# Performance work log

Measured on AMD Instinct MI355X. Metric: run time of the kernel, lower is better.

## Reference

```python
import jax, jax.numpy as jnp
import numpy as np

N = 100000   # nodes
E = 600000   # edges
D = 128      # hidden_dim
R = 8        # edge_vocab_size (num_relations)
B = 64       # graphs in batch
V = 5000     # node_vocab_size
L = 3        # num_layers


def setup_inputs() -> dict:
    key = jax.random.key(0)
    ks = jax.random.split(key, 16)
    s = 1.0 / np.sqrt(D)
    node_type = jax.random.randint(ks[0], (N,), 0, V, dtype=jnp.int32)
    edge_index = jax.random.randint(ks[1], (2, E), 0, N, dtype=jnp.int32)
    edge_type = jax.random.randint(ks[2], (E,), 0, R, dtype=jnp.int32)
    batch = jnp.sort(jax.random.randint(ks[3], (N,), 0, B, dtype=jnp.int32))
    node_emb = jax.random.normal(ks[4], (V, D), dtype=jnp.float32)
    rel_w = jax.random.normal(ks[5], (L, R, D, D), dtype=jnp.float32) * s
    root_w = jax.random.normal(ks[6], (L, D, D), dtype=jnp.float32) * s
    bias = jnp.zeros((L, D), dtype=jnp.float32)
    risk_w1 = jax.random.normal(ks[7], (D, D), dtype=jnp.float32) * s
    risk_b1 = jnp.zeros((D,), dtype=jnp.float32)
    risk_w2 = jax.random.normal(ks[8], (D, 1), dtype=jnp.float32) * s
    risk_b2 = jnp.zeros((1,), dtype=jnp.float32)
    safe_w1 = jax.random.normal(ks[9], (D, D), dtype=jnp.float32) * s
    safe_b1 = jnp.zeros((D,), dtype=jnp.float32)
    safe_w2 = jax.random.normal(ks[10], (D, 1), dtype=jnp.float32) * s
    safe_b2 = jnp.zeros((1,), dtype=jnp.float32)
    return dict(node_type=node_type, edge_index=edge_index, edge_type=edge_type,
                batch=batch, node_emb=node_emb, rel_w=rel_w, root_w=root_w,
                bias=bias, risk_w1=risk_w1, risk_b1=risk_b1, risk_w2=risk_w2,
                risk_b2=risk_b2, safe_w1=safe_w1, safe_b1=safe_b1,
                safe_w2=safe_w2, safe_b2=safe_b2)


def _rgcn_layer(x, edge_index, edge_type, Wrel, Wroot, b):
    # PyG RGCNConv: per-relation mean aggregation of source features,
    # then relation-specific linear + root transform + bias.
    src, dst = edge_index[0], edge_index[1]
    seg = dst * R + edge_type                      # combined (node, relation) id
    msgs = x[src]                                  # [E, D] gather
    sums = jax.ops.segment_sum(msgs, seg, num_segments=N * R)      # [N*R, D]
    cnt = jax.ops.segment_sum(jnp.ones((E,), x.dtype), seg, num_segments=N * R)
    mean = sums / jnp.maximum(cnt, 1.0)[:, None]
    mean = mean.reshape(N, R, D)
    out = jnp.einsum('nrd,rde->ne', mean, Wrel) + x @ Wroot + b
    return out


def _mlp_head(g, w1, b1, w2, b2):
    h = jax.nn.relu(g @ w1 + b1)
    return (h @ w2 + b2).squeeze(-1)               # dropout is identity in eval


def reference(node_type, edge_index, edge_type, batch, node_emb, rel_w, root_w,
              bias, risk_w1, risk_b1, risk_w2, risk_b2, safe_w1, safe_b1,
              safe_w2, safe_b2):
    x = node_emb[node_type]                        # [N, D]
    for l in range(L):                             # fixed small layer loop
        x = jax.nn.relu(_rgcn_layer(x, edge_index, edge_type,
                                    rel_w[l], root_w[l], bias[l]))
    # global_mean_pool over graph ids
    g_sum = jax.ops.segment_sum(x, batch, num_segments=B)          # [B, D]
    g_cnt = jax.ops.segment_sum(jnp.ones((N,), x.dtype), batch, num_segments=B)
    g = g_sum / jnp.maximum(g_cnt, 1.0)[:, None]
    risk_pred = _mlp_head(g, risk_w1, risk_b1, risk_w2, risk_b2)   # [B]
    safe_logit = _mlp_head(g, safe_w1, safe_b1, safe_w2, safe_b2)  # [B]
    return risk_pred, safe_logit
```

## Files before the change

kernel.cpp:

```cpp
#include <hip/hip_runtime.h>
#include <hip/hip_bf16.h>

#define N_NODES 100000
#define N_EDGES 600000
#define DIM     128
#define N_REL   8
#define N_GRAPH 64
#define N_LAYER 3
#define NR      (N_NODES * N_REL)
#define NB1     782

typedef __attribute__((ext_vector_type(4))) float float4v;
typedef __attribute__((ext_vector_type(2))) float float2v;
typedef unsigned long long ull;

__device__ __forceinline__ int gswz8(int row, int g) {
    return row * 16 + (g ^ (row & 15));
}

#define W8_TOTAL (N_LAYER * 9 * 8192)
#define PB_HIST  2344
#define PB_GATH  12500
#define PB_WPRE  864
#define PB_BCNT  1
#define PB_TOTAL (PB_HIST + PB_GATH + PB_WPRE + PB_BCNT)

__global__ __launch_bounds__(256) void k_prep(
    const int* __restrict__ ei, const int* __restrict__ et, int* __restrict__ counts,
    const int* __restrict__ nt, const float* __restrict__ emb, unsigned int* __restrict__ x8,
    const float* __restrict__ relw, const float* __restrict__ rootw,
    unsigned short* __restrict__ W8,
    const int* __restrict__ batch, int* __restrict__ gcnt)
{
    const int b = blockIdx.x, t = threadIdx.x;
    if (b < PB_HIST) {
        int e = b * 256 + t;
        if (e < N_EDGES) {
            int seg = ei[N_EDGES + e] * N_REL + et[e];
            atomicAdd(&counts[seg], 1);
        }
    } else if (b < PB_HIST + PB_GATH) {
        int gid = (b - PB_HIST) * 256 + t;
        int n = gid >> 5, up = gid & 31;
        const float* row = emb + (size_t)nt[n] * DIM;
        int p0 = up * 4;
        float f0 = row[((p0 + 0) & 7) * 16 + ((p0 + 0) >> 3)];
        float f1 = row[((p0 + 1) & 7) * 16 + ((p0 + 1) >> 3)];
        float f2 = row[((p0 + 2) & 7) * 16 + ((p0 + 2) >> 3)];
        float f3 = row[((p0 + 3) & 7) * 16 + ((p0 + 3) >> 3)];
        int u = __builtin_amdgcn_cvt_pk_fp8_f32(f0, f1, 0, false);
        u = __builtin_amdgcn_cvt_pk_fp8_f32(f2, f3, u, true);
        x8[gid] = (unsigned int)u;
    } else if (b < PB_HIST + PB_GATH + PB_WPRE) {
        int gid = (b - PB_HIST - PB_GATH) * 256 + t;
        int l = gid / (9 * 8192);
        int rem = gid - l * 9 * 8192;
        int r = rem >> 13;
        int idx = rem & 8191;
        int n = idx >> 6, p2 = idx & 63;
        int pos0 = 2 * p2, pos1 = 2 * p2 + 1;
        int k0 = (pos0 & 7) * 16 + (pos0 >> 3);
        int k1 = (pos1 & 7) * 16 + (pos1 >> 3);
        float w0, w1;
        if (r < 8) {
            const float* base = relw + ((size_t)(l * 8 + r) * 128) * 128 + n;
            w0 = base[(size_t)k0 * 128];
            w1 = base[(size_t)k1 * 128];
        } else {
            const float* base = rootw + (size_t)l * 128 * 128 + n;
            w0 = base[(size_t)k0 * 128];
            w1 = base[(size_t)k1 * 128];
        }
        int pk = __builtin_amdgcn_cvt_pk_fp8_f32(w0, w1, 0, false);
        W8[gid] = (unsigned short)(pk & 0xffff);
    } else {
        int g = t;
        if (g < N_GRAPH) {
            int lo = 0, hi = N_NODES;
            while (lo < hi) { int mid = (lo + hi) >> 1; if (batch[mid] < g) lo = mid + 1; else hi = mid; }
            int start = lo;
            lo = 0; hi = N_NODES;
            while (lo < hi) { int mid = (lo + hi) >> 1; if (batch[mid] < g + 1) lo = mid + 1; else hi = mid; }
            gcnt[g] = lo - start;
        }
    }
}

__global__ __launch_bounds__(256) void k_scan1(const int* __restrict__ cnts,
                                               int* __restrict__ part,
                                               int* __restrict__ bsum) {
    __shared__ int sh[256];
    int t = threadIdx.x;
    int base = blockIdx.x * 1024 + t * 4;
    int v0 = (base + 0 < NR) ? cnts[base + 0] : 0;
    int v1 = (base + 1 < NR) ? cnts[base + 1] : 0;
    int v2 = (base + 2 < NR) ? cnts[base + 2] : 0;
    int v3 = (base + 3 < NR) ? cnts[base + 3] : 0;
    int tot = v0 + v1 + v2 + v3;
    sh[t] = tot;
    __syncthreads();
    for (int off = 1; off < 256; off <<= 1) {
        int x = (t >= off) ? sh[t - off] : 0;
        __syncthreads();
        sh[t] += x;
        __syncthreads();
    }
    int exc = sh[t] - tot;
    if (base + 0 < NR) part[base + 0] = exc;
    if (base + 1 < NR) part[base + 1] = exc + v0;
    if (base + 2 < NR) part[base + 2] = exc + v0 + v1;
    if (base + 3 < NR) part[base + 3] = exc + v0 + v1 + v2;
    if (t == 255) bsum[blockIdx.x] = sh[t];
}

__global__ __launch_bounds__(1024) void k_scan2(int* __restrict__ bsum, int nb) {
    __shared__ int sh[1024];
    int t = threadIdx.x;
    int v = (t < nb) ? bsum[t] : 0;
    sh[t] = v;
    __syncthreads();
    for (int off = 1; off < 1024; off <<= 1) {
        int x = (t >= off) ? sh[t - off] : 0;
        __syncthreads();
        sh[t] += x;
        __syncthreads();
    }
    if (t < nb) bsum[t] = sh[t] - v;
}

__global__ void k_scan3(const int* __restrict__ part, const int* __restrict__ bsum,
                        int* __restrict__ rowptr, int* __restrict__ cursor) {
    int i = blockIdx.x * 256 + threadIdx.x;
    if (i < NR) {
        int v = part[i] + bsum[i >> 10];
        rowptr[i] = v;
        cursor[i] = v;
    }
    if (i == 0) rowptr[NR] = N_EDGES;
}

__global__ void k_scatter(const int* __restrict__ ei, const int* __restrict__ et,
                          int* __restrict__ cursor, int* __restrict__ srcs) {
    int e = blockIdx.x * 256 + threadIdx.x;
    if (e < N_EDGES) {
        int seg = ei[N_EDGES + e] * N_REL + et[e];
        int p = atomicAdd(&cursor[seg], 1);
        srcs[p] = ei[e];
    }
}

#define BM2 128
__global__ __launch_bounds__(256, 2) void k_gemm(
    const unsigned int* __restrict__ x8in,
    unsigned int* __restrict__ x8out,
    const unsigned short* __restrict__ W8,
    const float* __restrict__ bias,
    const int* __restrict__ rowptr,
    const int* __restrict__ srcs)
{
    __shared__ __align__(16) ull Bls[4096];
    __shared__ __align__(16) ull Als[2048];
    const int t = threadIdx.x;
    const int wv = t >> 6, lane = t & 63;
    const int quad = lane >> 4, l15 = lane & 15;
    const int oct = lane >> 3, h = lane & 7;
    const int m0 = blockIdx.x * BM2;
    const int gn = m0 + wv * 32 + (lane >> 1);
    const int f = lane & 1;

    float4v acc[2][8];
#pragma unroll
    for (int nt = 0; nt < 8; ++nt) {
        float bc = bias[nt * 16 + l15];
        acc[0][nt] = (float4v){bc, bc, bc, bc};
        acc[1][nt] = (float4v){bc, bc, bc, bc};
    }

    const ull* Xr = (const ull*)x8in;
    const uint4* x4p = (const uint4*)x8in;
    ull* AlsW = Als + wv * 512;
    uint4* Als4 = (uint4*)AlsW;

    ull bR[8], aR[8];
    uint4 u0[4], u1[4];
    int cc[4], eb[4], s2v[4], s3v[4];

#define ACCUM(U) do {                                                  \
        A0 += __builtin_amdgcn_cvt_pk_f32_fp8((int)(U).x, false);      \
        A1 += __builtin_amdgcn_cvt_pk_f32_fp8((int)(U).x, true);       \
        A2 += __builtin_amdgcn_cvt_pk_f32_fp8((int)(U).y, false);      \
        A3 += __builtin_amdgcn_cvt_pk_f32_fp8((int)(U).y, true);       \
        A4 += __builtin_amdgcn_cvt_pk_f32_fp8((int)(U).z, false);      \
        A5 += __builtin_amdgcn_cvt_pk_f32_fp8((int)(U).z, true);       \
        A6 += __builtin_amdgcn_cvt_pk_f32_fp8((int)(U).w, false);      \
        A7 += __builtin_amdgcn_cvt_pk_f32_fp8((int)(U).w, true);       \
    } while (0)

    auto rp_load = [&](int rr) -> int {
        int idxp = (gn < N_NODES) ? gn * 8 + rr + f : NR;
        return rowptr[idxp];
    };
    auto src_load = [&](int val, int& s0, int& s2) {
        int e0l = __shfl(val, lane & 62);
        int cl  = __shfl(val, lane | 1) - e0l;
        s0 = (f < cl) ? srcs[e0l + f] : 0;
        s2 = (f + 2 < cl) ? srcs[e0l + 2 + f] : 0;
    };
    auto gat_issue = [&](int val, int sl0, int sl2) {
#pragma unroll
        for (int nn = 0; nn < 4; ++nn) {
            int lw = nn * 8 + oct;
            int e0 = __shfl(val, lw * 2);
            int e1 = __shfl(val, lw * 2 + 1);
            cc[nn] = e1 - e0; eb[nn] = e0;
            int s0 = __shfl(sl0, lw * 2);
            int s1 = __shfl(sl0, lw * 2 + 1);
            s2v[nn] = __shfl(sl2, lw * 2);
            s3v[nn] = __shfl(sl2, lw * 2 + 1);
            if (cc[nn] > 0) u0[nn] = x4p[(size_t)s0 * 8 + h];
            if (cc[nn] > 1) u1[nn] = x4p[(size_t)s1 * 8 + h];
        }
    };
    auto agg_consume = [&]() {
        uint4 u2[4], u3[4];
#pragma unroll
        for (int nn = 0; nn < 4; ++nn) {
            if (cc[nn] > 2) u2[nn] = x4p[(size_t)s2v[nn] * 8 + h];
            if (cc[nn] > 3) u3[nn] = x4p[(size_t)s3v[nn] * 8 + h];
        }
#pragma unroll
        for (int nn = 0; nn < 4; ++nn) {
            int lw = nn * 8 + oct;
            float2v A0 = {0.f, 0.f}, A1 = {0.f, 0.f}, A2 = {0.f, 0.f}, A3 = {0.f, 0.f};
            float2v A4 = {0.f, 0.f}, A5 = {0.f, 0.f}, A6 = {0.f, 0.f}, A7 = {0.f, 0.f};
            if (cc[nn] > 0) ACCUM(u0[nn]);
            if (cc[nn] > 1) ACCUM(u1[nn]);
            if (cc[nn] > 2) ACCUM(u2[nn]);
            if (cc[nn] > 3) ACCUM(u3[nn]);
#pragma unroll 1
            for (int k = 4; k < cc[nn]; ++k) {
                int s = srcs[eb[nn] + k];
                uint4 uu = x4p[(size_t)s * 8 + h];
                ACCUM(uu);
            }
            float inv = (cc[nn] > 0) ? 1.0f / (float)cc[nn] : 0.f;
            float2v iv = {inv, inv};
            A0 *= iv; A1 *= iv; A2 *= iv; A3 *= iv;
            A4 *= iv; A5 *= iv; A6 *= iv; A7 *= iv;
            int w0 = __builtin_amdgcn_cvt_pk_fp8_f32(A0.x, A0.y, 0, false);
            w0 = __builtin_amdgcn_cvt_pk_fp8_f32(A1.x, A1.y, w0, true);
            int w1 = __builtin_amdgcn_cvt_pk_fp8_f32(A2.x, A2.y, 0, false);
            w1 = __builtin_amdgcn_cvt_pk_fp8_f32(A3.x, A3.y, w1, true);
            int w2 = __builtin_amdgcn_cvt_pk_fp8_f32(A4.x, A4.y, 0, false);
            w2 = __builtin_amdgcn_cvt_pk_fp8_f32(A5.x, A5.y, w2, true);
            int w3 = __builtin_amdgcn_cvt_pk_fp8_f32(A6.x, A6.y, 0, false);
            w3 = __builtin_amdgcn_cvt_pk_fp8_f32(A7.x, A7.y, w3, true);
            uint4 w; w.x = (unsigned int)w0; w.y = (unsigned int)w1;
            w.z = (unsigned int)w2; w.w = (unsigned int)w3;
            Als4[(lw >> 4) * 128 + h * 16 + ((lw & 15) ^ h)] = w;
        }
    };

    {
        const ull* Wc = (const ull*)W8;
#pragma unroll
        for (int i = 0; i < 8; ++i) bR[i] = Wc[t + 256 * i];
    }
    int vS3 = rp_load(0);
    int vS2 = rp_load(1);
    int vNew = rp_load(2);
    int sl0A, sl2A, sl0N, sl2N;
    src_load(vS3, sl0A, sl2A);
    gat_issue(vS3, sl0A, sl2A);
    src_load(vS2, sl0A, sl2A);
    agg_consume();
    vS3 = vS2; vS2 = vNew;
#pragma unroll
    for (int i = 0; i < 8; ++i) {
        int idx = t + 256 * i;
        Bls[gswz8(idx >> 4, idx & 15)] = bR[i];
    }
    __syncthreads();

#pragma unroll
    for (int c = 0; c < 9; ++c) {
        const int cur = (c & 1) * 2048;
        if (c <= 4) vNew = rp_load(c + 3);
        if (c <= 5) src_load(vS2, sl0N, sl2N);
        if (c <= 6) gat_issue(vS3, sl0A, sl2A);
        if (c < 8) {
            const ull* Wc = (const ull*)(W8 + (size_t)(c + 1) * 8192);
#pragma unroll
            for (int i = 0; i < 8; ++i) bR[i] = Wc[t + 256 * i];
        }
        if (c == 7) {
#pragma unroll
            for (int i = 0; i < 8; ++i) {
                int rt = i >> 2, kk = i & 3;
                aR[i] = Xr[(size_t)(m0 + wv * 32 + rt * 16 + l15) * 16 + kk * 4 + quad];
            }
        }
#pragma unroll
        for (int kk = 0; kk < 4; ++kk) {
            long long a0, a1;
            if (c == 8) {
                a0 = (long long)aR[kk];
                a1 = (long long)aR[4 + kk];
            } else {
                int j4 = kk * 4 + quad;
                int h2 = j4 >> 1, hf = j4 & 1;
                int slot = ((h2 * 16 + (l15 ^ h2)) << 1) | hf;
                a0 = (long long)AlsW[slot];
                a1 = (long long)AlsW[256 + slot];
            }
            int g = kk * 4 + quad;
#pragma unroll
            for (int nt = 0; nt < 8; ++nt) {
                long long b8 = (long long)Bls[cur + (nt * 16 + l15) * 16 + (g ^ l15)];
                acc[0][nt] = __builtin_amdgcn_mfma_f32_16x16x32_fp8_fp8(a0, b8, acc[0][nt], 0, 0, 0);
                acc[1][nt] = __builtin_amdgcn_mfma_f32_16x16x32_fp8_fp8(a1, b8, acc[1][nt], 0, 0, 0);
            }
        }
        if (c <= 6) agg_consume();
        if (c < 8) {
            const int nxt = ((c + 1) & 1) * 2048;
#pragma unroll
            for (int i = 0; i < 8; ++i) {
                int idx = t + 256 * i;
                Bls[nxt + gswz8(idx >> 4, idx & 15)] = bR[i];
            }
            __syncthreads();
        }
        vS3 = vS2; vS2 = vNew; sl0A = sl0N; sl2A = sl2N;
    }
#undef ACCUM

    ull* outs = (ull*)x8out;
#pragma unroll
    for (int rt = 0; rt < 2; ++rt) {
#pragma unroll
        for (int i = 0; i < 4; ++i) {
            int row = m0 + wv * 32 + rt * 16 + quad * 4 + i;
            float v0 = acc[rt][0][i], v1 = acc[rt][1][i];
            float v2 = acc[rt][2][i], v3 = acc[rt][3][i];
            float v4 = acc[rt][4][i], v5 = acc[rt][5][i];
            float v6 = acc[rt][6][i], v7 = acc[rt][7][i];
            v0 = v0 > 0.f ? v0 : 0.f;  v1 = v1 > 0.f ? v1 : 0.f;
            v2 = v2 > 0.f ? v2 : 0.f;  v3 = v3 > 0.f ? v3 : 0.f;
            v4 = v4 > 0.f ? v4 : 0.f;  v5 = v5 > 0.f ? v5 : 0.f;
            v6 = v6 > 0.f ? v6 : 0.f;  v7 = v7 > 0.f ? v7 : 0.f;
            int lo = __builtin_amdgcn_cvt_pk_fp8_f32(v0, v1, 0, false);
            lo = __builtin_amdgcn_cvt_pk_fp8_f32(v2, v3, lo, true);
            int hi = __builtin_amdgcn_cvt_pk_fp8_f32(v4, v5, 0, false);
            hi = __builtin_amdgcn_cvt_pk_fp8_f32(v6, v7, hi, true);
            if (row < N_NODES) {
                ull w = ((ull)(unsigned int)hi << 32) | (unsigned int)lo;
                outs[(size_t)row * 16 + l15] = w;
            }
        }
    }
}

__global__ __launch_bounds__(256) void k_pool(const unsigned int* __restrict__ x8,
                                              const int* __restrict__ batch,
                                              float* __restrict__ gsum) {
    const int wv = threadIdx.x >> 6, lane = threadIdx.x & 63;
    const int n0 = (blockIdx.x * 4 + wv) * 64;
    if (n0 >= N_NODES) return;
    int n1 = n0 + 64;
    if (n1 > N_NODES) n1 = N_NODES;
    const int nb = n1 - n0;
    const unsigned short* xs = (const unsigned short*)x8;
    int bb = batch[n0 + (lane < nb ? lane : nb - 1)];
    float2v A = {0.f, 0.f};
    int cur = __shfl(bb, 0);
    for (int base = 0; base < nb; base += 8) {
        unsigned int u[8];
        int m = nb - base;
#pragma unroll
        for (int qq = 0; qq < 8; ++qq)
            if (qq < m) u[qq] = xs[(size_t)(n0 + base + qq) * 64 + lane];
#pragma unroll
        for (int qq = 0; qq < 8; ++qq) {
            if (qq < m) {
                int b = __shfl(bb, base + qq);
                if (b != cur) {
                    atomicAdd(&gsum[cur * 128 + lane * 2], A.x);
                    atomicAdd(&gsum[cur * 128 + lane * 2 + 1], A.y);
                    A = (float2v){0.f, 0.f};
                    cur = b;
                }
                A += __builtin_amdgcn_cvt_pk_f32_fp8((int)u[qq], false);
            }
        }
    }
    atomicAdd(&gsum[cur * 128 + lane * 2], A.x);
    atomicAdd(&gsum[cur * 128 + lane * 2 + 1], A.y);
}

__global__ __launch_bounds__(128) void k_heads(
    const float* __restrict__ gsum, const int* __restrict__ gcnt,
    const float* __restrict__ rw1, const float* __restrict__ rb1,
    const float* __restrict__ rw2, const float* __restrict__ rb2,
    const float* __restrict__ sw1, const float* __restrict__ sb1,
    const float* __restrict__ sw2, const float* __restrict__ sb2,
    float* __restrict__ out) {
    __shared__ float g[128];
    __shared__ float parts[2];
    int b = blockIdx.x, t = threadIdx.x;
    int c = gcnt[b];
    float invc = 1.0f / (float)(c > 0 ? c : 1);
    g[((t & 7) << 4) | (t >> 3)] = gsum[b * 128 + t] * invc;
    __syncthreads();
    float acc = rb1[t];
    for (int d = 0; d < 128; ++d) acc += g[d] * rw1[d * 128 + t];
    float h = acc > 0.f ? acc : 0.f;
    float p = h * rw2[t];
    for (int o = 32; o > 0; o >>= 1) p += __shfl_down(p, o);
    if ((t & 63) == 0) parts[t >> 6] = p;
    __syncthreads();
    if (t == 0) out[b] = parts[0] + parts[1] + rb2[0];
    __syncthreads();
    acc = sb1[t];
    for (int d = 0; d < 128; ++d) acc += g[d] * sw1[d * 128 + t];
    h = acc > 0.f ? acc : 0.f;
    p = h * sw2[t];
    for (int o = 32; o > 0; o >>= 1) p += __shfl_down(p, o);
    if ((t & 63) == 0) parts[t >> 6] = p;
    __syncthreads();
    if (t == 0) out[64 + b] = parts[0] + parts[1] + sb2[0];
}

extern "C" void kernel_launch(void* const* d_in, const int* in_sizes, int n_in,
                              void* d_out, int out_size, void* d_ws, size_t ws_size,
                              hipStream_t stream) {
    const int*   node_type  = (const int*)d_in[0];
    const int*   edge_index = (const int*)d_in[1];
    const int*   edge_type  = (const int*)d_in[2];
    const int*   batch      = (const int*)d_in[3];
    const float* node_emb   = (const float*)d_in[4];
    const float* rel_w      = (const float*)d_in[5];
    const float* root_w     = (const float*)d_in[6];
    const float* bias       = (const float*)d_in[7];
    const float* rw1        = (const float*)d_in[8];
    const float* rb1        = (const float*)d_in[9];
    const float* rw2        = (const float*)d_in[10];
    const float* rb2        = (const float*)d_in[11];
    const float* sw1        = (const float*)d_in[12];
    const float* sb1        = (const float*)d_in[13];
    const float* sw2        = (const float*)d_in[14];
    const float* sb2        = (const float*)d_in[15];
    float* out = (float*)d_out;

    char* ws = (char*)d_ws;
    size_t off = 0;
    auto alloc = [&](size_t bytes) -> void* {
        void* p = ws + off;
        off += (bytes + 255) & ~(size_t)255;
        return p;
    };
    unsigned int*   x8a    = (unsigned int*)alloc((size_t)N_NODES * 32 * 4);
    unsigned int*   x8b    = (unsigned int*)alloc((size_t)N_NODES * 32 * 4);
    int*            rowptr = (int*)alloc((size_t)(NR + 1) * 4);
    int*            srcs   = (int*)alloc((size_t)N_EDGES * 4);
    int*            bsum   = (int*)alloc(1024 * 4);
    unsigned short* W8     = (unsigned short*)alloc((size_t)W8_TOTAL * 2);
    float*          gsum   = (float*)alloc((64 * 128 + 64) * 4);
    int*            gcnt   = (int*)(gsum + 64 * 128);
    int*            cursor = (int*)alloc((size_t)NR * 4);
    int*            counts = (int*)alloc((size_t)NR * 4);
    if (off > ws_size) return;

    hipMemsetAsync(counts, 0, (size_t)NR * 4, stream);
    hipMemsetAsync(gsum, 0, (size_t)(64 * 128 + 64) * 4, stream);
    k_prep<<<PB_TOTAL, 256, 0, stream>>>(edge_index, edge_type, counts,
                                         node_type, node_emb, x8a,
                                         rel_w, root_w, W8, batch, gcnt);
    k_scan1<<<NB1, 256, 0, stream>>>(counts, cursor, bsum);
    k_scan2<<<1, 1024, 0, stream>>>(bsum, NB1);
    k_scan3<<<(NR + 255) / 256, 256, 0, stream>>>(cursor, bsum, rowptr, cursor);
    k_scatter<<<(N_EDGES + 255) / 256, 256, 0, stream>>>(edge_index, edge_type, cursor, srcs);

    unsigned int* xcur = x8a;
    unsigned int* xnext = x8b;
    const int gb = (N_NODES + BM2 - 1) / BM2;
    for (int l = 0; l < N_LAYER; ++l) {
        const unsigned short* W8l = W8 + (size_t)l * 9 * 8192;
        const float* bl = bias + (size_t)l * 128;
        k_gemm<<<gb, 256, 0, stream>>>(xcur, xnext, W8l, bl, rowptr, srcs);
        unsigned int* tmp = xcur; xcur = xnext; xnext = tmp;
    }

    k_pool<<<(N_NODES + 255) / 256, 256, 0, stream>>>(xcur, batch, gsum);
    k_heads<<<64, 128, 0, stream>>>(gsum, gcnt, rw1, rb1, rw2, rb2,
                                    sw1, sb1, sw2, sb2, out);
}
```

Measured before the change: 388.3 us.

## Load FP8 weights directly into registers in MFMA fragment order, drop LDS staging

The weight prep kernel now writes each relation or root FP8 matrix already permuted into per-lane MFMA B-fragment order. The GEMM kernel reads those fragments straight from global memory (L2) into double-buffered registers, one k-step ahead, instead of staging them through a swizzled LDS double buffer with a barrier per chunk. This removes the LDS writes and reads and the block-wide __syncthreads in the weight path. In exchange every wave reloads the same weights from global or cache, which raises L2 traffic and register pressure under the 2-blocks-per-CU launch bound.

```diff
diff --git a/kernel.cpp b/kernel.cpp
--- a/kernel.cpp
+++ b/kernel.cpp
@@ -13,10 +13,6 @@
 typedef __attribute__((ext_vector_type(4))) float float4v;
 typedef __attribute__((ext_vector_type(2))) float float2v;
 typedef unsigned long long ull;
-
-__device__ __forceinline__ int gswz8(int row, int g) {
-    return row * 16 + (g ^ (row & 15));
-}
 
 #define W8_TOTAL (N_LAYER * 9 * 8192)
 #define PB_HIST  2344
@@ -55,15 +51,23 @@
         int gid = (b - PB_HIST - PB_GATH) * 256 + t;
         int l = gid / (9 * 8192);
         int rem = gid - l * 9 * 8192;
-        int r = rem >> 13;
+        int c = rem >> 13;
         int idx = rem & 8191;
-        int n = idx >> 6, p2 = idx & 63;
+        int pp = idx & 3;
+        int fu = idx >> 2;
+        int lane = fu & 63;
+        int kkNt = fu >> 6;
+        int kk = kkNt >> 3, ntc = kkNt & 7;
+        int quad = lane >> 4, l15 = lane & 15;
+        int n = ntc * 16 + l15;
+        int g = kk * 4 + quad;
+        int p2 = g * 4 + pp;
         int pos0 = 2 * p2, pos1 = 2 * p2 + 1;
         int k0 = (pos0 & 7) * 16 + (pos0 >> 3);
         int k1 = (pos1 & 7) * 16 + (pos1 >> 3);
         float w0, w1;
-        if (r < 8) {
-            const float* base = relw + ((size_t)(l * 8 + r) * 128) * 128 + n;
+        if (c < 8) {
+            const float* base = relw + ((size_t)(l * 8 + c) * 128) * 128 + n;
             w0 = base[(size_t)k0 * 128];
             w1 = base[(size_t)k1 * 128];
         } else {
@@ -150,6 +154,7 @@
 }
 
 #define BM2 128
+#define WCH 2048
 __global__ __launch_bounds__(256, 2) void k_gemm(
     const unsigned int* __restrict__ x8in,
     unsigned int* __restrict__ x8out,
@@ -158,7 +163,6 @@
     const int* __restrict__ rowptr,
     const int* __restrict__ srcs)
 {
-    __shared__ __align__(16) ull Bls[4096];
     __shared__ __align__(16) ull Als[2048];
     const int t = threadIdx.x;
     const int wv = t >> 6, lane = t & 63;
@@ -168,6 +172,14 @@
     const int gn = m0 + wv * 32 + (lane >> 1);
     const int f = lane & 1;
 
+    const ull* Wf = (const ull*)W8;
+
+    ull bW0[8], bW1[8];
+    {
+#pragma unroll
+        for (int i = 0; i < 8; ++i) bW0[i] = Wf[(i << 6) + lane];
+    }
+
     float4v acc[2][8];
 #pragma unroll
     for (int nt = 0; nt < 8; ++nt) {
@@ -181,7 +193,7 @@
     ull* AlsW = Als + wv * 512;
     uint4* Als4 = (uint4*)AlsW;
 
-    ull bR[8], aR[8];
+    ull aR[8];
     uint4 u0[4], u1[4];
     int cc[4], eb[4], s2v[4], s3v[4];
 
@@ -261,11 +273,6 @@
         }
     };
 
-    {
-        const ull* Wc = (const ull*)W8;
-#pragma unroll
-        for (int i = 0; i < 8; ++i) bR[i] = Wc[t + 256 * i];
-    }
     int vS3 = rp_load(0);
     int vS2 = rp_load(1);
     int vNew = rp_load(2);
@@ -275,24 +282,12 @@
     src_load(vS2, sl0A, sl2A);
     agg_consume();
     vS3 = vS2; vS2 = vNew;
-#pragma unroll
-    for (int i = 0; i < 8; ++i) {
-        int idx = t + 256 * i;
-        Bls[gswz8(idx >> 4, idx & 15)] = bR[i];
-    }
-    __syncthreads();
 
 #pragma unroll
     for (int c = 0; c < 9; ++c) {
-        const int cur = (c & 1) * 2048;
         if (c <= 4) vNew = rp_load(c + 3);
         if (c <= 5) src_load(vS2, sl0N, sl2N);
         if (c <= 6) gat_issue(vS3, sl0A, sl2A);
-        if (c < 8) {
-            const ull* Wc = (const ull*)(W8 + (size_t)(c + 1) * 8192);
-#pragma unroll
-            for (int i = 0; i < 8; ++i) bR[i] = Wc[t + 256 * i];
-        }
         if (c == 7) {
 #pragma unroll
             for (int i = 0; i < 8; ++i) {
@@ -302,6 +297,20 @@
         }
 #pragma unroll
         for (int kk = 0; kk < 4; ++kk) {
+            if (kk < 3) {
+                const ull* Wc = Wf + (size_t)c * WCH + (((kk + 1) * 8) << 6);
+                if (((kk + 1) & 1) == 0) {
+#pragma unroll
+                    for (int i = 0; i < 8; ++i) bW0[i] = Wc[(i << 6) + lane];
+                } else {
+#pragma unroll
+                    for (int i = 0; i < 8; ++i) bW1[i] = Wc[(i << 6) + lane];
+                }
+            } else if (c < 8) {
+                const ull* Wc = Wf + (size_t)(c + 1) * WCH;
+#pragma unroll
+                for (int i = 0; i < 8; ++i) bW0[i] = Wc[(i << 6) + lane];
+            }
             long long a0, a1;
             if (c == 8) {
                 a0 = (long long)aR[kk];
@@ -313,24 +322,21 @@
                 a0 = (long long)AlsW[slot];
                 a1 = (long long)AlsW[256 + slot];
             }
-            int g = kk * 4 + quad;
-#pragma unroll
-            for (int nt = 0; nt < 8; ++nt) {
-                long long b8 = (long long)Bls[cur + (nt * 16 + l15) * 16 + (g ^ l15)];
-                acc[0][nt] = __builtin_amdgcn_mfma_f32_16x16x32_fp8_fp8(a0, b8, acc[0][nt], 0, 0, 0);
-                acc[1][nt] = __builtin_amdgcn_mfma_f32_16x16x32_fp8_fp8(a1, b8, acc[1][nt], 0, 0, 0);
+            if ((kk & 1) == 0) {
+#pragma unroll
+                for (int nt = 0; nt < 8; ++nt) {
+                    acc[0][nt] = __builtin_amdgcn_mfma_f32_16x16x32_fp8_fp8(a0, (long long)bW0[nt], acc[0][nt], 0, 0, 0);
+                    acc[1][nt] = __builtin_amdgcn_mfma_f32_16x16x32_fp8_fp8(a1, (long long)bW0[nt], acc[1][nt], 0, 0, 0);
+                }
+            } else {
+#pragma unroll
+                for (int nt = 0; nt < 8; ++nt) {
+                    acc[0][nt] = __builtin_amdgcn_mfma_f32_16x16x32_fp8_fp8(a0, (long long)bW1[nt], acc[0][nt], 0, 0, 0);
+                    acc[1][nt] = __builtin_amdgcn_mfma_f32_16x16x32_fp8_fp8(a1, (long long)bW1[nt], acc[1][nt], 0, 0, 0);
+                }
             }
         }
         if (c <= 6) agg_consume();
-        if (c < 8) {
-            const int nxt = ((c + 1) & 1) * 2048;
-#pragma unroll
-            for (int i = 0; i < 8; ++i) {
-                int idx = t + 256 * i;
-                Bls[nxt + gswz8(idx >> 4, idx & 15)] = bR[i];
-            }
-            __syncthreads();
-        }
         vS3 = vS2; vS2 = vNew; sl0A = sl0N; sl2A = sl2N;
     }
 #undef ACCUM
```

Measured after the change: 403.3 us. +3.9%, slower.

## Replace CSR scan/scatter with fixed 4-slot buckets and overflow list

Applied to the files above, without the earlier changes.

The prep kernel now fills a per-(node,relation) array of up to four source slots and a count, using atomics. Edges beyond the fourth go to a global overflow list. This removes the three scan kernels and the scatter kernel, and the gemm reads counts and source slots directly instead of the rowptr/srcs indirection. Segments with more than four edges are handled by a linear scan of the whole overflow list, which is divergent and costly, and edges past OVF_CAP would be silently dropped. The aggregation call is also moved ahead of the MFMA step in the pipeline.

```diff
diff --git a/kernel.cpp b/kernel.cpp
--- a/kernel.cpp
+++ b/kernel.cpp
@@ -8,7 +8,7 @@
 #define N_GRAPH 64
 #define N_LAYER 3
 #define NR      (N_NODES * N_REL)
-#define NB1     782
+#define OVF_CAP 131072
 
 typedef __attribute__((ext_vector_type(4))) float float4v;
 typedef __attribute__((ext_vector_type(2))) float float2v;
@@ -26,7 +26,9 @@
 #define PB_TOTAL (PB_HIST + PB_GATH + PB_WPRE + PB_BCNT)
 
 __global__ __launch_bounds__(256) void k_prep(
-    const int* __restrict__ ei, const int* __restrict__ et, int* __restrict__ counts,
+    const int* __restrict__ ei, const int* __restrict__ et,
+    int* __restrict__ cnt, int* __restrict__ srcs4,
+    int* __restrict__ ovf, int* __restrict__ ovf_n,
     const int* __restrict__ nt, const float* __restrict__ emb, unsigned int* __restrict__ x8,
     const float* __restrict__ relw, const float* __restrict__ rootw,
     unsigned short* __restrict__ W8,
@@ -36,8 +38,15 @@
     if (b < PB_HIST) {
         int e = b * 256 + t;
         if (e < N_EDGES) {
+            int src = ei[e];
             int seg = ei[N_EDGES + e] * N_REL + et[e];
-            atomicAdd(&counts[seg], 1);
+            int p = atomicAdd(&cnt[seg], 1);
+            if (p < 4) {
+                srcs4[seg * 4 + p] = src;
+            } else {
+                int q = atomicAdd(ovf_n, 1);
+                if (q < OVF_CAP) { ovf[2 * q] = seg; ovf[2 * q + 1] = src; }
+            }
         }
     } else if (b < PB_HIST + PB_GATH) {
         int gid = (b - PB_HIST) * 256 + t;
@@ -86,77 +95,16 @@
     }
 }
 
-__global__ __launch_bounds__(256) void k_scan1(const int* __restrict__ cnts,
-                                               int* __restrict__ part,
-                                               int* __restrict__ bsum) {
-    __shared__ int sh[256];
-    int t = threadIdx.x;
-    int base = blockIdx.x * 1024 + t * 4;
-    int v0 = (base + 0 < NR) ? cnts[base + 0] : 0;
-    int v1 = (base + 1 < NR) ? cnts[base + 1] : 0;
-    int v2 = (base + 2 < NR) ? cnts[base + 2] : 0;
-    int v3 = (base + 3 < NR) ? cnts[base + 3] : 0;
-    int tot = v0 + v1 + v2 + v3;
-    sh[t] = tot;
-    __syncthreads();
-    for (int off = 1; off < 256; off <<= 1) {
-        int x = (t >= off) ? sh[t - off] : 0;
-        __syncthreads();
-        sh[t] += x;
-        __syncthreads();
-    }
-    int exc = sh[t] - tot;
-    if (base + 0 < NR) part[base + 0] = exc;
-    if (base + 1 < NR) part[base + 1] = exc + v0;
-    if (base + 2 < NR) part[base + 2] = exc + v0 + v1;
-    if (base + 3 < NR) part[base + 3] = exc + v0 + v1 + v2;
-    if (t == 255) bsum[blockIdx.x] = sh[t];
-}
-
-__global__ __launch_bounds__(1024) void k_scan2(int* __restrict__ bsum, int nb) {
-    __shared__ int sh[1024];
-    int t = threadIdx.x;
-    int v = (t < nb) ? bsum[t] : 0;
-    sh[t] = v;
-    __syncthreads();
-    for (int off = 1; off < 1024; off <<= 1) {
-        int x = (t >= off) ? sh[t - off] : 0;
-        __syncthreads();
-        sh[t] += x;
-        __syncthreads();
-    }
-    if (t < nb) bsum[t] = sh[t] - v;
-}
-
-__global__ void k_scan3(const int* __restrict__ part, const int* __restrict__ bsum,
-                        int* __restrict__ rowptr, int* __restrict__ cursor) {
-    int i = blockIdx.x * 256 + threadIdx.x;
-    if (i < NR) {
-        int v = part[i] + bsum[i >> 10];
-        rowptr[i] = v;
-        cursor[i] = v;
-    }
-    if (i == 0) rowptr[NR] = N_EDGES;
-}
-
-__global__ void k_scatter(const int* __restrict__ ei, const int* __restrict__ et,
-                          int* __restrict__ cursor, int* __restrict__ srcs) {
-    int e = blockIdx.x * 256 + threadIdx.x;
-    if (e < N_EDGES) {
-        int seg = ei[N_EDGES + e] * N_REL + et[e];
-        int p = atomicAdd(&cursor[seg], 1);
-        srcs[p] = ei[e];
-    }
-}
-
 #define BM2 128
 __global__ __launch_bounds__(256, 2) void k_gemm(
     const unsigned int* __restrict__ x8in,
     unsigned int* __restrict__ x8out,
     const unsigned short* __restrict__ W8,
     const float* __restrict__ bias,
-    const int* __restrict__ rowptr,
-    const int* __restrict__ srcs)
+    const int* __restrict__ cnt,
+    const int* __restrict__ srcs4,
+    const int* __restrict__ ovf,
+    const int* __restrict__ ovf_n)
 {
     __shared__ __align__(16) ull Bls[4096];
     __shared__ __align__(16) ull Als[2048];
@@ -166,6 +114,7 @@
     const int oct = lane >> 3, h = lane & 7;
     const int m0 = blockIdx.x * BM2;
     const int gn = m0 + wv * 32 + (lane >> 1);
+    const int nodeC = (gn < N_NODES) ? gn : 0;
     const int f = lane & 1;
 
     float4v acc[2][8];
@@ -183,7 +132,7 @@
 
     ull bR[8], aR[8];
     uint4 u0[4], u1[4];
-    int cc[4], eb[4], s2v[4], s3v[4];
+    int cc[4], s2v[4], s3v[4];
 
 #define ACCUM(U) do {                                                  \
         A0 += __builtin_amdgcn_cvt_pk_f32_fp8((int)(U).x, false);      \
@@ -196,23 +145,17 @@
         A7 += __builtin_amdgcn_cvt_pk_f32_fp8((int)(U).w, true);       \
     } while (0)
 
-    auto rp_load = [&](int rr) -> int {
-        int idxp = (gn < N_NODES) ? gn * 8 + rr + f : NR;
-        return rowptr[idxp];
+    auto ld_meta = [&](int rr, int& cl, int& s0, int& s2) {
+        int seg = nodeC * 8 + rr;
+        cl = cnt[seg];
+        s0 = srcs4[seg * 4 + f];
+        s2 = srcs4[seg * 4 + 2 + f];
     };
-    auto src_load = [&](int val, int& s0, int& s2) {
-        int e0l = __shfl(val, lane & 62);
-        int cl  = __shfl(val, lane | 1) - e0l;
-        s0 = (f < cl) ? srcs[e0l + f] : 0;
-        s2 = (f + 2 < cl) ? srcs[e0l + 2 + f] : 0;
-    };
-    auto gat_issue = [&](int val, int sl0, int sl2) {
+    auto gat_issue = [&](int cl, int sl0, int sl2) {
 #pragma unroll
         for (int nn = 0; nn < 4; ++nn) {
             int lw = nn * 8 + oct;
-            int e0 = __shfl(val, lw * 2);
-            int e1 = __shfl(val, lw * 2 + 1);
-            cc[nn] = e1 - e0; eb[nn] = e0;
+            cc[nn] = __shfl(cl, lw * 2);
             int s0 = __shfl(sl0, lw * 2);
             int s1 = __shfl(sl0, lw * 2 + 1);
             s2v[nn] = __shfl(sl2, lw * 2);
@@ -221,7 +164,7 @@
             if (cc[nn] > 1) u1[nn] = x4p[(size_t)s1 * 8 + h];
         }
     };
-    auto agg_consume = [&]() {
+    auto agg_consume = [&](int rr) {
         uint4 u2[4], u3[4];
 #pragma unroll
         for (int nn = 0; nn < 4; ++nn) {
@@ -237,11 +180,17 @@
             if (cc[nn] > 1) ACCUM(u1[nn]);
             if (cc[nn] > 2) ACCUM(u2[nn]);
             if (cc[nn] > 3) ACCUM(u3[nn]);
+            if (cc[nn] > 4) {
+                int seg = (m0 + wv * 32 + lw) * 8 + rr;
+                int ovn = ovf_n[0];
+                if (ovn > OVF_CAP) ovn = OVF_CAP;
 #pragma unroll 1
-            for (int k = 4; k < cc[nn]; ++k) {
-                int s = srcs[eb[nn] + k];
-                uint4 uu = x4p[(size_t)s * 8 + h];
-                ACCUM(uu);
+                for (int j = 0; j < ovn; ++j) {
+                    if (ovf[2 * j] == seg) {
+                        uint4 uu = x4p[(size_t)ovf[2 * j + 1] * 8 + h];
+                        ACCUM(uu);
+                    }
+                }
             }
             float inv = (cc[nn] > 0) ? 1.0f / (float)cc[nn] : 0.f;
             float2v iv = {inv, inv};
@@ -266,15 +215,10 @@
 #pragma unroll
         for (int i = 0; i < 8; ++i) bR[i] = Wc[t + 256 * i];
     }
-    int vS3 = rp_load(0);
-    int vS2 = rp_load(1);
-    int vNew = rp_load(2);
-    int sl0A, sl2A, sl0N, sl2N;
-    src_load(vS3, sl0A, sl2A);
-    gat_issue(vS3, sl0A, sl2A);
-    src_load(vS2, sl0A, sl2A);
-    agg_consume();
-    vS3 = vS2; vS2 = vNew;
+    int clA, sl0A, sl2A, clN, sl0N, sl2N;
+    ld_meta(0, clA, sl0A, sl2A);
+    gat_issue(clA, sl0A, sl2A);
+    ld_meta(1, clA, sl0A, sl2A);
 #pragma unroll
     for (int i = 0; i < 8; ++i) {
         int idx = t + 256 * i;
@@ -285,9 +229,9 @@
 #pragma unroll
     for (int c = 0; c < 9; ++c) {
         const int cur = (c & 1) * 2048;
-        if (c <= 4) vNew = rp_load(c + 3);
-        if (c <= 5) src_load(vS2, sl0N, sl2N);
-        if (c <= 6) gat_issue(vS3, sl0A, sl2A);
+        if (c <= 7) agg_consume(c);
+        if (c <= 5) ld_meta(c + 2, clN, sl0N, sl2N);
+        if (c <= 6) gat_issue(clA, sl0A, sl2A);
         if (c < 8) {
             const ull* Wc = (const ull*)(W8 + (size_t)(c + 1) * 8192);
 #pragma unroll
@@ -321,7 +265,6 @@
                 acc[1][nt] = __builtin_amdgcn_mfma_f32_16x16x32_fp8_fp8(a1, b8, acc[1][nt], 0, 0, 0);
             }
         }
-        if (c <= 6) agg_consume();
         if (c < 8) {
             const int nxt = ((c + 1) & 1) * 2048;
 #pragma unroll
@@ -331,7 +274,7 @@
             }
             __syncthreads();
         }
-        vS3 = vS2; vS2 = vNew; sl0A = sl0N; sl2A = sl2N;
+        clA = clN; sl0A = sl0N; sl2A = sl2N;
     }
 #undef ACCUM
 
@@ -461,25 +404,20 @@
     };
     unsigned int*   x8a    = (unsigned int*)alloc((size_t)N_NODES * 32 * 4);
     unsigned int*   x8b    = (unsigned int*)alloc((size_t)N_NODES * 32 * 4);
-    int*            rowptr = (int*)alloc((size_t)(NR + 1) * 4);
-    int*            srcs   = (int*)alloc((size_t)N_EDGES * 4);
-    int*            bsum   = (int*)alloc(1024 * 4);
+    int*            cnt    = (int*)alloc((size_t)NR * 4);
+    int*            srcs4  = (int*)alloc((size_t)NR * 4 * 4);
+    int*            ovf    = (int*)alloc((size_t)OVF_CAP * 2 * 4);
     unsigned short* W8     = (unsigned short*)alloc((size_t)W8_TOTAL * 2);
-    float*          gsum   = (float*)alloc((64 * 128 + 64) * 4);
+    float*          gsum   = (float*)alloc((64 * 128 + 64 + 64) * 4);
     int*            gcnt   = (int*)(gsum + 64 * 128);
-    int*            cursor = (int*)alloc((size_t)NR * 4);
-    int*            counts = (int*)alloc((size_t)NR * 4);
+    int*            ovf_n  = (int*)(gsum + 64 * 128 + 64);
     if (off > ws_size) return;
 
-    hipMemsetAsync(counts, 0, (size_t)NR * 4, stream);
-    hipMemsetAsync(gsum, 0, (size_t)(64 * 128 + 64) * 4, stream);
-    k_prep<<<PB_TOTAL, 256, 0, stream>>>(edge_index, edge_type, counts,
+    hipMemsetAsync(cnt, 0, (size_t)NR * 4, stream);
+    hipMemsetAsync(gsum, 0, (size_t)(64 * 128 + 64 + 64) * 4, stream);
+    k_prep<<<PB_TOTAL, 256, 0, stream>>>(edge_index, edge_type, cnt, srcs4, ovf, ovf_n,
                                          node_type, node_emb, x8a,
                                          rel_w, root_w, W8, batch, gcnt);
-    k_scan1<<<NB1, 256, 0, stream>>>(counts, cursor, bsum);
-    k_scan2<<<1, 1024, 0, stream>>>(bsum, NB1);
-    k_scan3<<<(NR + 255) / 256, 256, 0, stream>>>(cursor, bsum, rowptr, cursor);
-    k_scatter<<<(N_EDGES + 255) / 256, 256, 0, stream>>>(edge_index, edge_type, cursor, srcs);
 
     unsigned int* xcur = x8a;
     unsigned int* xnext = x8b;
@@ -487,7 +425,7 @@
     for (int l = 0; l < N_LAYER; ++l) {
         const unsigned short* W8l = W8 + (size_t)l * 9 * 8192;
         const float* bl = bias + (size_t)l * 128;
-        k_gemm<<<gb, 256, 0, stream>>>(xcur, xnext, W8l, bl, rowptr, srcs);
+        k_gemm<<<gb, 256, 0, stream>>>(xcur, xnext, W8l, bl, cnt, srcs4, ovf, ovf_n);
         unsigned int* tmp = xcur; xcur = xnext; xnext = tmp;
     }
 
```

After: 1.421 ms. +265.9%, slower.
